# Performance work log

Hardware: AMD Instinct MI355X
Metric: run time of the kernel (lower is better)

Reference implementation:

```python
import jax, jax.numpy as jnp
import numpy as np


def _make_window():
    g = jnp.array([0.0113, 0.0838, 0.0113], dtype=jnp.float32)
    w = jnp.outer(g, g)  # [3,3]
    return w[None, None, :, :]  # [O=1, I=1, 3, 3]


def _conv(x, w):
    # x: [B,1,H,W], w: [1,1,3,3]; padding=1 -> SAME for 3x3
    return jax.lax.conv_general_dilated(
        x, w, window_strides=(1, 1), padding=((1, 1), (1, 1)),
        dimension_numbers=('NCHW', 'OIHW', 'NCHW'))


def setup_inputs() -> dict:
    key = jax.random.key(0)
    k1, k2 = jax.random.split(key)
    shape = (64, 1, 480, 640)
    x = jax.random.uniform(k1, shape, dtype=jnp.float32)
    y = jax.random.uniform(k2, shape, dtype=jnp.float32)
    return {"x": x, "y": y}


def reference(x, y):
    w = _make_window().astype(x.dtype)
    mu_x = _conv(x, w)
    mu_y = _conv(y, w)
    sigma_x = _conv(x * x, w) - mu_x * mu_x
    sigma_y = _conv(y * y, w) - mu_y * mu_y
    sigma_xy = _conv(x * y, w) - mu_x * mu_y
    C1, C2 = 0.01 ** 2, 0.03 ** 2
    ssim = (2 * mu_x * mu_y + C1) * (2 * sigma_xy + C2) / (
        (mu_x * mu_x + mu_y * mu_y + C1) * (sigma_x + sigma_y + C2))
    return 1.0 - ssim.mean()
```

## Files before the change

### kernel.cpp

```cpp
#include <hip/hip_runtime.h>


#define IMG_H 480
#define IMG_W 640
#define IMG_B 64
#define NPIX (IMG_B * IMG_H * IMG_W)
#define ROWS 10
#define STRIPS (IMG_H / ROWS)
#define QCOLS (IMG_W / 4)
#define NTH 256
#define NITEMS (IMG_B * STRIPS * QCOLS)
#define NBLK (NITEMS / NTH)
#define FTH 256

__device__ __forceinline__ float4 f4z() { return make_float4(0.f, 0.f, 0.f, 0.f); }
__device__ __forceinline__ float4 f4s(float s, float4 a) {
    return make_float4(s * a.x, s * a.y, s * a.z, s * a.w);
}
__device__ __forceinline__ float4 f4fma(float s, float4 a, float4 b) {
    return make_float4(fmaf(s, a.x, b.x), fmaf(s, a.y, b.y),
                       fmaf(s, a.z, b.z), fmaf(s, a.w, b.w));
}

__device__ __forceinline__ void hfilt4(const float* __restrict__ xp,
                                       const float* __restrict__ yp,
                                       bool has_l, bool has_r,
                                       float4& mx, float4& my,
                                       float4& sxx, float4& syy, float4& sxy) {
    const float g0 = 0.0113f, g1 = 0.0838f;
    const float4 x4 = *(const float4*)xp;
    const float4 y4 = *(const float4*)yp;
    const float xa = has_l ? xp[-1] : 0.0f;
    const float xb = has_r ? xp[4]  : 0.0f;
    const float ya = has_l ? yp[-1] : 0.0f;
    const float yb = has_r ? yp[4]  : 0.0f;

    mx = make_float4(g0 * (xa + x4.y) + g1 * x4.x,
                     g0 * (x4.x + x4.z) + g1 * x4.y,
                     g0 * (x4.y + x4.w) + g1 * x4.z,
                     g0 * (x4.z + xb) + g1 * x4.w);
    my = make_float4(g0 * (ya + y4.y) + g1 * y4.x,
                     g0 * (y4.x + y4.z) + g1 * y4.y,
                     g0 * (y4.y + y4.w) + g1 * y4.z,
                     g0 * (y4.z + yb) + g1 * y4.w);

    const float qxa = xa * xa, qx0 = x4.x * x4.x, qx1 = x4.y * x4.y;
    const float qx2 = x4.z * x4.z, qx3 = x4.w * x4.w, qxb = xb * xb;
    sxx = make_float4(g0 * (qxa + qx1) + g1 * qx0,
                      g0 * (qx0 + qx2) + g1 * qx1,
                      g0 * (qx1 + qx3) + g1 * qx2,
                      g0 * (qx2 + qxb) + g1 * qx3);

    const float qya = ya * ya, qy0 = y4.x * y4.x, qy1 = y4.y * y4.y;
    const float qy2 = y4.z * y4.z, qy3 = y4.w * y4.w, qyb = yb * yb;
    syy = make_float4(g0 * (qya + qy1) + g1 * qy0,
                      g0 * (qy0 + qy2) + g1 * qy1,
                      g0 * (qy1 + qy3) + g1 * qy2,
                      g0 * (qy2 + qyb) + g1 * qy3);

    const float pa = xa * ya, p0 = x4.x * y4.x, p1 = x4.y * y4.y;
    const float p2 = x4.z * y4.z, p3 = x4.w * y4.w, pb = xb * yb;
    sxy = make_float4(g0 * (pa + p1) + g1 * p0,
                      g0 * (p0 + p2) + g1 * p1,
                      g0 * (p1 + p3) + g1 * p2,
                      g0 * (p2 + pb) + g1 * p3);
}

__device__ __forceinline__ float ssim4(float4 mx, float4 my, float4 xx,
                                       float4 yy, float4 xy) {
    const float C1 = 1e-4f, C2 = 9e-4f;
    float acc = 0.0f;
#define SSIM1(MX, MY, XX, YY, XY)                                         \
    {                                                                     \
        const float sx = (XX) - (MX) * (MX);                              \
        const float sy = (YY) - (MY) * (MY);                              \
        const float sxy_ = (XY) - (MX) * (MY);                            \
        const float num = (2.0f * (MX) * (MY) + C1) * (2.0f * sxy_ + C2); \
        const float den = ((MX) * (MX) + (MY) * (MY) + C1) *              \
                          (sx + sy + C2);                                 \
        acc += num * __builtin_amdgcn_rcpf(den);                          \
    }
    SSIM1(mx.x, my.x, xx.x, yy.x, xy.x)
    SSIM1(mx.y, my.y, xx.y, yy.y, xy.y)
    SSIM1(mx.z, my.z, xx.z, yy.z, xy.z)
    SSIM1(mx.w, my.w, xx.w, yy.w, xy.w)
#undef SSIM1
    return acc;
}

__global__ __launch_bounds__(NTH) void ssim_partial_kernel(
        const float* __restrict__ x, const float* __restrict__ y,
        float* __restrict__ partials) {
    const float g0 = 0.0113f, g1 = 0.0838f;

    const int tid = blockIdx.x * NTH + threadIdx.x;
    const int c = tid % QCOLS;
    const int t = tid / QCOLS;
    const int s = t % STRIPS;
    const int b = t / STRIPS;

    const bool has_l = (c > 0);
    const bool has_r = (c < QCOLS - 1);
    const int h0 = s * ROWS;

    const size_t img = (size_t)IMG_H * IMG_W;
    const float* xp = x + (size_t)b * img + (size_t)(h0 - 1) * IMG_W + 4 * c;
    const float* yp = y + (size_t)b * img + (size_t)(h0 - 1) * IMG_W + 4 * c;

    float4 P1mx = f4z(), P1my = f4z(), P1xx = f4z(), P1yy = f4z(), P1xy = f4z();
    float4 P2mx = f4z(), P2my = f4z(), P2xx = f4z(), P2yy = f4z(), P2xy = f4z();

    if (h0 > 0) {
        float4 fmx, fmy, fxx, fyy, fxy;
        hfilt4(xp, yp, has_l, has_r, fmx, fmy, fxx, fyy, fxy);
        P2mx = f4s(g0, fmx); P2my = f4s(g0, fmy);
        P2xx = f4s(g0, fxx); P2yy = f4s(g0, fyy); P2xy = f4s(g0, fxy);
    }
    xp += IMG_W; yp += IMG_W;

    float local = 0.0f;
#pragma unroll 2
    for (int it = 1; it <= ROWS + 1; ++it) {
        const int hin = h0 - 1 + it;
        float4 fmx, fmy, fxx, fyy, fxy;
        if (hin < IMG_H) {
            hfilt4(xp, yp, has_l, has_r, fmx, fmy, fxx, fyy, fxy);
        } else {
            fmx = fmy = fxx = fyy = fxy = f4z();
        }

        if (it >= 2) {
            const float4 omx = f4fma(g0, fmx, P1mx);
            const float4 omy = f4fma(g0, fmy, P1my);
            const float4 oxx = f4fma(g0, fxx, P1xx);
            const float4 oyy = f4fma(g0, fyy, P1yy);
            const float4 oxy = f4fma(g0, fxy, P1xy);
            local += ssim4(omx, omy, oxx, oyy, oxy);
        }

        P1mx = f4fma(g1, fmx, P2mx); P1my = f4fma(g1, fmy, P2my);
        P1xx = f4fma(g1, fxx, P2xx); P1yy = f4fma(g1, fyy, P2yy);
        P1xy = f4fma(g1, fxy, P2xy);
        P2mx = f4s(g0, fmx); P2my = f4s(g0, fmy);
        P2xx = f4s(g0, fxx); P2yy = f4s(g0, fyy); P2xy = f4s(g0, fxy);

        xp += IMG_W; yp += IMG_W;
    }

    for (int off = 32; off > 0; off >>= 1)
        local += __shfl_down(local, off, 64);
    __shared__ float sred[NTH / 64];
    const int lane = threadIdx.x & 63;
    const int wid  = threadIdx.x >> 6;
    if (lane == 0) sred[wid] = local;
    __syncthreads();
    if (threadIdx.x == 0) {
        float t0 = 0.0f;
#pragma unroll
        for (int i = 0; i < NTH / 64; ++i) t0 += sred[i];
        partials[blockIdx.x] = t0;
    }
}

__global__ void ssim_finalize_kernel(const float* __restrict__ partials,
                                     float* __restrict__ out) {
    double acc = 0.0;
    for (int i = threadIdx.x; i < NBLK; i += FTH)
        acc += (double)partials[i];
    __shared__ double s[FTH];
    s[threadIdx.x] = acc;
    __syncthreads();
    for (int off = FTH / 2; off > 0; off >>= 1) {
        if (threadIdx.x < off) s[threadIdx.x] += s[threadIdx.x + off];
        __syncthreads();
    }
    if (threadIdx.x == 0) {
        const double mean = s[0] / (double)NPIX;
        out[0] = (float)(1.0 - mean);
    }
}

extern "C" void kernel_launch(void* const* d_in, const int* in_sizes, int n_in,
                              void* d_out, int out_size, void* d_ws, size_t ws_size,
                              hipStream_t stream) {
    const float* x = (const float*)d_in[0];
    const float* y = (const float*)d_in[1];
    float* partials = (float*)d_ws;
    float* out = (float*)d_out;

    ssim_partial_kernel<<<NBLK, NTH, 0, stream>>>(x, y, partials);
    ssim_finalize_kernel<<<1, FTH, 0, stream>>>(partials, out);
}
```

Before: 187.1 us.

## Prefetch next row into registers and enlarge strip height

Restructures the row loop to load the next row's raw x/y values before filtering the current one, using clamped, branchless loads and a validity mask instead of conditional loads. The last output row is peeled into an epilogue. Strip height rises from 10 to 15 rows to reduce the halo reload overhead per output. The deeper software pipeline raises register pressure, and taller strips cut the total thread count, which may reduce latency hiding.

Result: faster. 178.5 us (-4.6%).

```diff
diff --git a/kernel.cpp b/kernel.cpp
--- a/kernel.cpp
+++ b/kernel.cpp
@@ -5,7 +5,7 @@
 #define IMG_W 640
 #define IMG_B 64
 #define NPIX (IMG_B * IMG_H * IMG_W)
-#define ROWS 10
+#define ROWS 15
 #define STRIPS (IMG_H / ROWS)
 #define QCOLS (IMG_W / 4)
 #define NTH 256
@@ -13,6 +13,8 @@
 #define NBLK (NITEMS / NTH)
 #define FTH 256
 
+struct Raw { float4 x4, y4; float xa, xb, ya, yb; };
+
 __device__ __forceinline__ float4 f4z() { return make_float4(0.f, 0.f, 0.f, 0.f); }
 __device__ __forceinline__ float4 f4s(float s, float4 a) {
     return make_float4(s * a.x, s * a.y, s * a.z, s * a.w);
@@ -22,44 +24,55 @@
                        fmaf(s, a.z, b.z), fmaf(s, a.w, b.w));
 }
 
-__device__ __forceinline__ void hfilt4(const float* __restrict__ xp,
-                                       const float* __restrict__ yp,
-                                       bool has_l, bool has_r,
-                                       float4& mx, float4& my,
-                                       float4& sxx, float4& syy, float4& sxy) {
+__device__ __forceinline__ void load_raw(const float* __restrict__ xp,
+                                         const float* __restrict__ yp,
+                                         int off_l, int off_r, Raw& r) {
+    r.x4 = *(const float4*)xp;
+    r.y4 = *(const float4*)yp;
+    r.xa = xp[off_l];
+    r.xb = xp[off_r];
+    r.ya = yp[off_l];
+    r.yb = yp[off_r];
+}
+
+__device__ __forceinline__ void hfilt4m(const Raw& r, bool v, bool has_l, bool has_r,
+                                        float4& mx, float4& my,
+                                        float4& sxx, float4& syy, float4& sxy) {
     const float g0 = 0.0113f, g1 = 0.0838f;
-    const float4 x4 = *(const float4*)xp;
-    const float4 y4 = *(const float4*)yp;
-    const float xa = has_l ? xp[-1] : 0.0f;
-    const float xb = has_r ? xp[4]  : 0.0f;
-    const float ya = has_l ? yp[-1] : 0.0f;
-    const float yb = has_r ? yp[4]  : 0.0f;
-
-    mx = make_float4(g0 * (xa + x4.y) + g1 * x4.x,
-                     g0 * (x4.x + x4.z) + g1 * x4.y,
-                     g0 * (x4.y + x4.w) + g1 * x4.z,
-                     g0 * (x4.z + xb) + g1 * x4.w);
-    my = make_float4(g0 * (ya + y4.y) + g1 * y4.x,
-                     g0 * (y4.x + y4.z) + g1 * y4.y,
-                     g0 * (y4.y + y4.w) + g1 * y4.z,
-                     g0 * (y4.z + yb) + g1 * y4.w);
-
-    const float qxa = xa * xa, qx0 = x4.x * x4.x, qx1 = x4.y * x4.y;
-    const float qx2 = x4.z * x4.z, qx3 = x4.w * x4.w, qxb = xb * xb;
+    const float x0 = v ? r.x4.x : 0.f, x1 = v ? r.x4.y : 0.f;
+    const float x2 = v ? r.x4.z : 0.f, x3 = v ? r.x4.w : 0.f;
+    const float y0 = v ? r.y4.x : 0.f, y1 = v ? r.y4.y : 0.f;
+    const float y2 = v ? r.y4.z : 0.f, y3 = v ? r.y4.w : 0.f;
+    const float xa = (v && has_l) ? r.xa : 0.f;
+    const float xb = (v && has_r) ? r.xb : 0.f;
+    const float ya = (v && has_l) ? r.ya : 0.f;
+    const float yb = (v && has_r) ? r.yb : 0.f;
+
+    mx = make_float4(g0 * (xa + x1) + g1 * x0,
+                     g0 * (x0 + x2) + g1 * x1,
+                     g0 * (x1 + x3) + g1 * x2,
+                     g0 * (x2 + xb) + g1 * x3);
+    my = make_float4(g0 * (ya + y1) + g1 * y0,
+                     g0 * (y0 + y2) + g1 * y1,
+                     g0 * (y1 + y3) + g1 * y2,
+                     g0 * (y2 + yb) + g1 * y3);
+
+    const float qxa = xa * xa, qx0 = x0 * x0, qx1 = x1 * x1;
+    const float qx2 = x2 * x2, qx3 = x3 * x3, qxb = xb * xb;
     sxx = make_float4(g0 * (qxa + qx1) + g1 * qx0,
                       g0 * (qx0 + qx2) + g1 * qx1,
                       g0 * (qx1 + qx3) + g1 * qx2,
                       g0 * (qx2 + qxb) + g1 * qx3);
 
-    const float qya = ya * ya, qy0 = y4.x * y4.x, qy1 = y4.y * y4.y;
-    const float qy2 = y4.z * y4.z, qy3 = y4.w * y4.w, qyb = yb * yb;
+    const float qya = ya * ya, qy0 = y0 * y0, qy1 = y1 * y1;
+    const float qy2 = y2 * y2, qy3 = y3 * y3, qyb = yb * yb;
     syy = make_float4(g0 * (qya + qy1) + g1 * qy0,
                       g0 * (qy0 + qy2) + g1 * qy1,
                       g0 * (qy1 + qy3) + g1 * qy2,
                       g0 * (qy2 + qyb) + g1 * qy3);
 
-    const float pa = xa * ya, p0 = x4.x * y4.x, p1 = x4.y * y4.y;
-    const float p2 = x4.z * y4.z, p3 = x4.w * y4.w, pb = xb * yb;
+    const float pa = xa * ya, p0 = x0 * y0, p1 = x1 * y1;
+    const float p2 = x2 * y2, p3 = x3 * y3, pb = xb * yb;
     sxy = make_float4(g0 * (pa + p1) + g1 * p0,
                       g0 * (p0 + p2) + g1 * p1,
                       g0 * (p1 + p3) + g1 * p2,
@@ -101,35 +114,38 @@
 
     const bool has_l = (c > 0);
     const bool has_r = (c < QCOLS - 1);
+    const int off_l = has_l ? -1 : 0;
+    const int off_r = has_r ? 4 : 3;
     const int h0 = s * ROWS;
 
     const size_t img = (size_t)IMG_H * IMG_W;
-    const float* xp = x + (size_t)b * img + (size_t)(h0 - 1) * IMG_W + 4 * c;
-    const float* yp = y + (size_t)b * img + (size_t)(h0 - 1) * IMG_W + 4 * c;
+    const float* xb0 = x + (size_t)b * img + 4 * c;
+    const float* yb0 = y + (size_t)b * img + 4 * c;
 
     float4 P1mx = f4z(), P1my = f4z(), P1xx = f4z(), P1yy = f4z(), P1xy = f4z();
     float4 P2mx = f4z(), P2my = f4z(), P2xx = f4z(), P2yy = f4z(), P2xy = f4z();
 
-    if (h0 > 0) {
-        float4 fmx, fmy, fxx, fyy, fxy;
-        hfilt4(xp, yp, has_l, has_r, fmx, fmy, fxx, fyy, fxy);
-        P2mx = f4s(g0, fmx); P2my = f4s(g0, fmy);
-        P2xx = f4s(g0, fxx); P2yy = f4s(g0, fyy); P2xy = f4s(g0, fxy);
-    }
-    xp += IMG_W; yp += IMG_W;
+    Raw cur, nxt;
+    {
+        const int r0 = (h0 > 0) ? (h0 - 1) : 0;
+        load_raw(xb0 + (size_t)r0 * IMG_W, yb0 + (size_t)r0 * IMG_W,
+                 off_l, off_r, cur);
+    }
+    bool vcur = (h0 > 0);
 
     float local = 0.0f;
 #pragma unroll 2
-    for (int it = 1; it <= ROWS + 1; ++it) {
-        const int hin = h0 - 1 + it;
+    for (int j = 0; j <= ROWS; ++j) {
+        const int hn = h0 + j;
+        const int rn = (hn < IMG_H) ? hn : (IMG_H - 1);
+        load_raw(xb0 + (size_t)rn * IMG_W, yb0 + (size_t)rn * IMG_W,
+                 off_l, off_r, nxt);
+        const bool vnxt = (hn < IMG_H);
+
         float4 fmx, fmy, fxx, fyy, fxy;
-        if (hin < IMG_H) {
-            hfilt4(xp, yp, has_l, has_r, fmx, fmy, fxx, fyy, fxy);
-        } else {
-            fmx = fmy = fxx = fyy = fxy = f4z();
-        }
-
-        if (it >= 2) {
+        hfilt4m(cur, vcur, has_l, has_r, fmx, fmy, fxx, fyy, fxy);
+
+        if (j >= 2) {
             const float4 omx = f4fma(g0, fmx, P1mx);
             const float4 omy = f4fma(g0, fmy, P1my);
             const float4 oxx = f4fma(g0, fxx, P1xx);
@@ -144,7 +160,18 @@
         P2mx = f4s(g0, fmx); P2my = f4s(g0, fmy);
         P2xx = f4s(g0, fxx); P2yy = f4s(g0, fyy); P2xy = f4s(g0, fxy);
 
-        xp += IMG_W; yp += IMG_W;
+        cur = nxt; vcur = vnxt;
+    }
+
+    {
+        float4 fmx, fmy, fxx, fyy, fxy;
+        hfilt4m(cur, vcur, has_l, has_r, fmx, fmy, fxx, fyy, fxy);
+        const float4 omx = f4fma(g0, fmx, P1mx);
+        const float4 omy = f4fma(g0, fmy, P1my);
+        const float4 oxx = f4fma(g0, fxx, P1xx);
+        const float4 oyy = f4fma(g0, fyy, P1yy);
+        const float4 oxy = f4fma(g0, fxy, P1xy);
+        local += ssim4(omx, omy, oxx, oyy, oxy);
     }
 
     for (int off = 32; off > 0; off >>= 1)
```
